# Kernel optimization log

Hardware: AMD Instinct MI355X
Metric: run time of the kernel (lower is better)

Reference implementation:

```python
import jax, jax.numpy as jnp
import numpy as np

D_K = 64
ATTN_MASKED = True
NEG = 1.0e9


def setup_inputs() -> dict:
    key = jax.random.key(0)
    k1, k2, k3, k4 = jax.random.split(key, 4)
    B, H, S, d = 2, 16, 2048, D_K
    Q = jax.random.normal(k1, (B, H, S, d), dtype=jnp.float32)
    K = jax.random.normal(k2, (B, H, S, d), dtype=jnp.float32)
    V = jax.random.normal(k3, (B, H, S, d), dtype=jnp.float32)
    pad_mask = jax.random.randint(k4, (B, S), 0, 2, dtype=jnp.int32)
    return {"Q": Q, "K": K, "V": V, "pad_mask": pad_mask}


def reference(Q, K, V, pad_mask):
    # scores: [B, H, Sq, Sk]
    scores = jnp.einsum("bhqd,bhkd->bhqk", Q, K) / np.sqrt(D_K).astype(np.float32)
    S_out, S_in = scores.shape[-2], scores.shape[-1]
    pad = pad_mask[:, None, None, :].astype(scores.dtype)  # [B,1,1,Sk]
    if ATTN_MASKED:
        causal = jnp.triu(jnp.ones((S_out, S_in), dtype=scores.dtype), k=1)[None, None]
        mask = ((pad + causal) > 0).astype(scores.dtype)
    else:
        mask = jnp.broadcast_to(pad, scores.shape)
    scores = scores - NEG * mask
    attn = jax.nn.softmax(scores, axis=-1)
    return jnp.einsum("bhqk,bhkd->bhqd", attn, V)
```

## Files before the change

### kernel.cpp

```cpp
#include <hip/hip_runtime.h>
#include <hip/hip_bf16.h>

#define S_LEN 2048
#define DH    64
#define NBH   32
#define QT    128
#define KVT   64

typedef __attribute__((ext_vector_type(8)))  short short8;
typedef __attribute__((ext_vector_type(4)))  float f32x4;
typedef __attribute__((ext_vector_type(16))) float f32x16;

static __device__ __forceinline__ unsigned cvtpk_bf16(float a, float b) {
    unsigned r;
    asm("v_cvt_pk_bf16_f32 %0, %1, %2" : "=v"(r) : "v"(a), "v"(b));
    return r;
}

__global__ __launch_bounds__(256)
void attn_fwd(const float* __restrict__ Q, const float* __restrict__ K,
              const float* __restrict__ V, const int* __restrict__ pad,
              float* __restrict__ out)
{
    __shared__ __align__(16) char  ldsK[2][KVT * 128];
    __shared__ __align__(16) char  ldsV[2][DH * 128];
    __shared__ __align__(16) float ldsPB[2][KVT];

    const int tid  = threadIdx.x;
    const int lane = tid & 63;
    const int wid  = tid >> 6;
    const int bx   = gridDim.x - 1 - blockIdx.x;
    const int bh   = blockIdx.y;
    const int b    = bh >> 4;

    const int q0   = bx * QT;
    const int q0w  = q0 + wid * 32;
    const long base = (long)bh * S_LEN * DH;

    const int lq = lane & 31;
    const int hi = lane >> 5;

    const float QS = 0.18033688011112042f;
    short8 bq[4];
    {
        const float* qp = Q + base + (long)(q0w + lq) * DH;
        #pragma unroll
        for (int s = 0; s < 4; ++s) {
            int d0 = s * 16 + hi * 8;
            f32x4 x = *(const f32x4*)(qp + d0);
            f32x4 y = *(const f32x4*)(qp + d0 + 4);
            union { short8 s8; unsigned u[4]; } u;
            u.u[0] = cvtpk_bf16(x[0] * QS, x[1] * QS);
            u.u[1] = cvtpk_bf16(x[2] * QS, x[3] * QS);
            u.u[2] = cvtpk_bf16(y[0] * QS, y[1] * QS);
            u.u[3] = cvtpk_bf16(y[2] * QS, y[3] * QS);
            bq[s] = u.s8;
        }
    }

    f32x16 o0, o1;
    #pragma unroll
    for (int r = 0; r < 16; ++r) { o0[r] = 0.f; o1[r] = 0.f; }
    float m_run = -1e30f, l_run = 0.f;

    const int nkv = 2 * (bx + 1);

    f32x4 kst[4], vst[4];
    int   pst = 0;
    const int vdg = tid & 15, vkq = tid >> 4;
    const float* Kb = K + base;
    const float* Vb = V + base;

    auto stage_load = [&](int t) {
        const float* kp = Kb + t * (KVT * DH);
        #pragma unroll
        for (int i = 0; i < 4; ++i)
            kst[i] = *(const f32x4*)(kp + i * 1024 + tid * 4);
        const float* vp = Vb + t * (KVT * DH);
        #pragma unroll
        for (int j = 0; j < 4; ++j)
            vst[j] = *(const f32x4*)(vp + (vkq * 4 + j) * DH + vdg * 4);
        pst = pad[b * S_LEN + t * KVT + (tid & 63)];
    };
    auto stage_write = [&](int buf) {
        char* kB = ldsK[buf];
        #pragma unroll
        for (int i = 0; i < 4; ++i) {
            int f = i * 1024 + tid * 4;
            int row = f >> 6, dc = f & 63;
            unsigned lo = cvtpk_bf16(kst[i][0], kst[i][1]);
            unsigned h2 = cvtpk_bf16(kst[i][2], kst[i][3]);
            int ch = (dc >> 3) ^ (row & 7);
            *(uint2*)(kB + row * 128 + ch * 16 + (dc & 7) * 2) = make_uint2(lo, h2);
        }
        char* vB = ldsV[buf];
        #pragma unroll
        for (int i = 0; i < 4; ++i) {
            int d = vdg * 4 + i;
            unsigned lo = cvtpk_bf16(vst[0][i], vst[1][i]);
            unsigned h2 = cvtpk_bf16(vst[2][i], vst[3][i]);
            int ch = (vkq >> 1) ^ (d & 7);
            *(uint2*)(vB + d * 128 + ch * 16 + (vkq & 1) * 8) = make_uint2(lo, h2);
        }
        if (tid < KVT) ldsPB[buf][tid] = pst ? -1e30f : 0.f;
    };

    stage_load(0);
    stage_write(0);
    __syncthreads();

    for (int t = 0; t < nkv; ++t) {
        const int cur = t & 1;
        const int kv0 = t * KVT;
        if (t + 1 < nkv) stage_load(t + 1);

        if (kv0 <= q0w + 31) {
            const char*  kB = ldsK[cur];
            const char*  vB = ldsV[cur];
            const float* pb = ldsPB[cur];
            const int    rsw = lq & 7;

            f32x16 s0, s1;
            #pragma unroll
            for (int g = 0; g < 4; ++g) {
                f32x4 p0 = *(const f32x4*)(pb + g * 8 + hi * 4);
                f32x4 p1 = *(const f32x4*)(pb + 32 + g * 8 + hi * 4);
                #pragma unroll
                for (int i = 0; i < 4; ++i) { s0[g * 4 + i] = p0[i]; s1[g * 4 + i] = p1[i]; }
            }

            __builtin_amdgcn_s_setprio(1);
            #pragma unroll
            for (int s = 0; s < 4; ++s) {
                int ch = (((s * 2 + hi) ^ rsw) * 16);
                short8 ak0 = *(const short8*)(kB + lq * 128 + ch);
                short8 ak1 = *(const short8*)(kB + (32 + lq) * 128 + ch);
                s0 = __builtin_amdgcn_mfma_f32_32x32x16_bf16(ak0, bq[s], s0, 0, 0, 0);
                s1 = __builtin_amdgcn_mfma_f32_32x32x16_bf16(ak1, bq[s], s1, 0, 0, 0);
            }
            __builtin_amdgcn_s_setprio(0);

            if (kv0 + 63 > q0w) {
                int q = q0w + lq;
                #pragma unroll
                for (int r = 0; r < 16; ++r) {
                    int key0 = kv0 + (r & 3) + 8 * (r >> 2) + 4 * hi;
                    if (key0 > q)      s0[r] = -1e30f;
                    if (key0 + 32 > q) s1[r] = -1e30f;
                }
            }

            float bm = -1e30f;
            #pragma unroll
            for (int r = 0; r < 16; ++r) bm = fmaxf(bm, fmaxf(s0[r], s1[r]));
            bm = fmaxf(bm, __shfl_xor(bm, 32));
            if (__any(bm > m_run + 8.0f)) {
                float mnew = fmaxf(m_run, bm);
                float c = exp2f(m_run - mnew);
                m_run = mnew;
                l_run *= c;
                #pragma unroll
                for (int r = 0; r < 16; ++r) { o0[r] *= c; o1[r] *= c; }
            }
            float rs = 0.f;
            #pragma unroll
            for (int r = 0; r < 16; ++r) {
                float p0 = exp2f(s0[r] - m_run);
                float p1 = exp2f(s1[r] - m_run);
                s0[r] = p0; s1[r] = p1;
                rs += p0 + p1;
            }
            rs += __shfl_xor(rs, 32);
            l_run += rs;

            short8 pfr[4];
            #pragma unroll
            for (int fs = 0; fs < 4; ++fs) {
                const f32x16& sp = (fs < 2) ? s0 : s1;
                const int rb = (fs & 1) * 8;
                unsigned a0 = cvtpk_bf16(sp[rb + 0], sp[rb + 1]);
                unsigned b0 = cvtpk_bf16(sp[rb + 4], sp[rb + 5]);
                asm("v_permlane32_swap_b32 %0, %1" : "+v"(a0), "+v"(b0));
                unsigned a1 = cvtpk_bf16(sp[rb + 2], sp[rb + 3]);
                unsigned b1 = cvtpk_bf16(sp[rb + 6], sp[rb + 7]);
                asm("v_permlane32_swap_b32 %0, %1" : "+v"(a1), "+v"(b1));
                union { short8 s8; unsigned u[4]; } u;
                u.u[0] = a0; u.u[1] = a1; u.u[2] = b0; u.u[3] = b1;
                pfr[fs] = u.s8;
            }

            __builtin_amdgcn_s_setprio(1);
            #pragma unroll
            for (int fs = 0; fs < 4; ++fs) {
                int ch = (((fs * 2 + hi) ^ rsw) * 16);
                short8 av0 = *(const short8*)(vB + lq * 128 + ch);
                short8 av1 = *(const short8*)(vB + (32 + lq) * 128 + ch);
                o0 = __builtin_amdgcn_mfma_f32_32x32x16_bf16(av0, pfr[fs], o0, 0, 0, 0);
                o1 = __builtin_amdgcn_mfma_f32_32x32x16_bf16(av1, pfr[fs], o1, 0, 0, 0);
            }
            __builtin_amdgcn_s_setprio(0);
        }

        if (t + 1 < nkv) stage_write((t + 1) & 1);
        __syncthreads();
    }

    float invl = 1.0f / l_run;
    float* op = out + base + (long)(q0w + lq) * DH;
    #pragma unroll
    for (int g = 0; g < 4; ++g) {
        f32x4 w0, w1;
        #pragma unroll
        for (int i = 0; i < 4; ++i) {
            w0[i] = o0[g * 4 + i] * invl;
            w1[i] = o1[g * 4 + i] * invl;
        }
        *(f32x4*)(op + g * 8 + hi * 4)      = w0;
        *(f32x4*)(op + 32 + g * 8 + hi * 4) = w1;
    }
}

__global__ void fz_kernel(const int* __restrict__ pad, int* __restrict__ fz)
{
    int b = blockIdx.x;
    __shared__ int red[256];
    int local = S_LEN;
    for (int k = threadIdx.x; k < S_LEN; k += 256)
        if (pad[b * S_LEN + k] == 0 && k < local) local = k;
    red[threadIdx.x] = local;
    __syncthreads();
    for (int s = 128; s > 0; s >>= 1) {
        if (threadIdx.x < s) red[threadIdx.x] = min(red[threadIdx.x], red[threadIdx.x + s]);
        __syncthreads();
    }
    if (threadIdx.x == 0) fz[b] = red[0];
}

__global__ __launch_bounds__(1024)
void meanv_kernel(const float* __restrict__ V, const int* __restrict__ fz,
                  float* __restrict__ meanv)
{
    const int bh = blockIdx.x;
    const int b  = bh >> 4;
    if (fz[b] <= 0) return;

    const int d4 = threadIdx.x & 15;
    const int kp = threadIdx.x >> 4;
    const float* vp = V + (long)bh * S_LEN * DH;

    f32x4 acc = (f32x4){0.f, 0.f, 0.f, 0.f};
    #pragma unroll 4
    for (int k = kp; k < S_LEN; k += 64)
        acc += *(const f32x4*)(vp + (long)k * DH + d4 * 4);

    __shared__ f32x4 red[64][16];
    red[kp][d4] = acc;
    __syncthreads();
    #pragma unroll
    for (int s = 32; s >= 1; s >>= 1) {
        if (kp < s) red[kp][d4] += red[kp + s][d4];
        __syncthreads();
    }
    if (kp == 0) {
        f32x4 m = red[0][d4] * (1.0f / 2048.0f);
        *(f32x4*)(meanv + bh * DH + d4 * 4) = m;
    }
}

__global__ void fixup_kernel(const int* __restrict__ fz, const float* __restrict__ meanv,
                             float* __restrict__ out)
{
    const int bh = blockIdx.x;
    const int b  = bh >> 4;
    const int n  = fz[b];
    if (n <= 0) return;

    __shared__ float mv[DH];
    if (threadIdx.x < DH) mv[threadIdx.x] = meanv[bh * DH + threadIdx.x];
    __syncthreads();

    float* op = out + (long)bh * S_LEN * DH;
    for (int i = threadIdx.x; i < n * DH; i += 256) op[i] = mv[i & 63];
}

extern "C" void kernel_launch(void* const* d_in, const int* in_sizes, int n_in,
                              void* d_out, int out_size, void* d_ws, size_t ws_size,
                              hipStream_t stream)
{
    const float* Q   = (const float*)d_in[0];
    const float* K   = (const float*)d_in[1];
    const float* V   = (const float*)d_in[2];
    const int*   pad = (const int*)d_in[3];
    float* out   = (float*)d_out;
    int*   fz    = (int*)d_ws;
    float* meanv = (float*)((char*)d_ws + 256);

    fz_kernel<<<dim3(2), dim3(256), 0, stream>>>(pad, fz);
    attn_fwd<<<dim3(S_LEN / QT, NBH), dim3(256), 0, stream>>>(Q, K, V, pad, out);
    meanv_kernel<<<dim3(NBH), dim3(1024), 0, stream>>>(V, fz, meanv);
    fixup_kernel<<<dim3(NBH), dim3(256), 0, stream>>>(fz, meanv, out);
}
```

Measured before the change: 107.5 us.

## Pre-convert K/V to swizzled bf16 tiles and stream via global_load_lds

Adds a prep kernel that converts K and V once into bf16 tiles already in the swizzled LDS layout, plus a kernel that precomputes the pad bias. The attention kernel then copies those tiles straight into LDS with global_load_lds instead of loading fp32, converting and writing through registers. It also remaps the grid so heavy and light causal blocks are interleaved. The cost is extra launches, workspace traffic, and a full vmcnt wait before each barrier. It only takes this path when the workspace is large enough, otherwise it falls back to the old kernel.

```diff
diff --git a/kernel.cpp b/kernel.cpp
--- a/kernel.cpp
+++ b/kernel.cpp
@@ -6,6 +6,7 @@
 #define NBH   32
 #define QT    128
 #define KVT   64
+#define NTILE 32
 
 typedef __attribute__((ext_vector_type(8)))  short short8;
 typedef __attribute__((ext_vector_type(4)))  float f32x4;
@@ -17,10 +18,75 @@
     return r;
 }
 
+typedef __attribute__((address_space(1))) const void gvoid_t;
+typedef __attribute__((address_space(3))) void lvoid_t;
+static __device__ __forceinline__ void gload16(const void* g, void* l) {
+    __builtin_amdgcn_global_load_lds((gvoid_t*)g, (lvoid_t*)l, 16, 0, 0);
+}
+static __device__ __forceinline__ void gload4(const void* g, void* l) {
+    __builtin_amdgcn_global_load_lds((gvoid_t*)g, (lvoid_t*)l, 4, 0, 0);
+}
+
 __global__ __launch_bounds__(256)
-void attn_fwd(const float* __restrict__ Q, const float* __restrict__ K,
-              const float* __restrict__ V, const int* __restrict__ pad,
-              float* __restrict__ out)
+void prep_kernel(const float* __restrict__ K, const float* __restrict__ V,
+                 char* __restrict__ Kimg, char* __restrict__ Vimg)
+{
+    const int t   = blockIdx.x;
+    const int bh  = blockIdx.y;
+    const int tid = threadIdx.x;
+    const long tileOff = ((long)bh * NTILE + t) * 8192;
+    const long srcOff  = (long)bh * S_LEN * DH + (long)t * KVT * DH;
+
+    {
+        const float* kp = K + srcOff;
+        char* dst = Kimg + tileOff;
+        #pragma unroll
+        for (int i = 0; i < 4; ++i) {
+            int f = i * 1024 + tid * 4;
+            int row = f >> 6, dc = f & 63;
+            f32x4 x = *(const f32x4*)(kp + f);
+            unsigned lo = cvtpk_bf16(x[0], x[1]);
+            unsigned h2 = cvtpk_bf16(x[2], x[3]);
+            int ch = (dc >> 3) ^ (row & 7);
+            *(uint2*)(dst + row * 128 + ch * 16 + (dc & 7) * 2) = make_uint2(lo, h2);
+        }
+    }
+    {
+        const float* vp = V + srcOff;
+        char* dst = Vimg + tileOff;
+        const int vdg = tid & 15, vkq = tid >> 4;
+        float rv[4][4];
+        #pragma unroll
+        for (int j = 0; j < 4; ++j) {
+            f32x4 x = *(const f32x4*)(vp + (vkq * 4 + j) * DH + vdg * 4);
+            rv[j][0] = x[0]; rv[j][1] = x[1]; rv[j][2] = x[2]; rv[j][3] = x[3];
+        }
+        #pragma unroll
+        for (int i = 0; i < 4; ++i) {
+            int d = vdg * 4 + i;
+            unsigned lo = cvtpk_bf16(rv[0][i], rv[1][i]);
+            unsigned h2 = cvtpk_bf16(rv[2][i], rv[3][i]);
+            int ch = (vkq >> 1) ^ (d & 7);
+            *(uint2*)(dst + d * 128 + ch * 16 + (vkq & 1) * 8) = make_uint2(lo, h2);
+        }
+    }
+}
+
+__global__ __launch_bounds__(1024)
+void bias_kernel(const int* __restrict__ pad, float* __restrict__ bias)
+{
+    int b = blockIdx.x;
+    #pragma unroll
+    for (int i = 0; i < 2; ++i) {
+        int k = threadIdx.x + i * 1024;
+        bias[b * S_LEN + k] = pad[b * S_LEN + k] ? -1e30f : 0.f;
+    }
+}
+
+__global__ __launch_bounds__(256)
+void attn_fwd2(const float* __restrict__ Q, const char* __restrict__ Kimg,
+               const char* __restrict__ Vimg, const float* __restrict__ bias,
+               float* __restrict__ out)
 {
     __shared__ __align__(16) char  ldsK[2][KVT * 128];
     __shared__ __align__(16) char  ldsV[2][DH * 128];
@@ -29,12 +95,15 @@
     const int tid  = threadIdx.x;
     const int lane = tid & 63;
     const int wid  = tid >> 6;
-    const int bx   = gridDim.x - 1 - blockIdx.x;
-    const int bh   = blockIdx.y;
+
+    const int gid  = blockIdx.x;
+    const int half = gid >> 8;
+    const int r    = gid & 255;
+    const int bx   = half ? (r & 15) : 15 - (r & 15);
+    const int bh   = (r >> 4) + (half << 4);
     const int b    = bh >> 4;
 
-    const int q0   = bx * QT;
-    const int q0w  = q0 + wid * 32;
+    const int q0w  = bx * QT + wid * 32;
     const long base = (long)bh * S_LEN * DH;
 
     const int lq = lane & 31;
@@ -60,59 +129,43 @@
 
     f32x16 o0, o1;
     #pragma unroll
-    for (int r = 0; r < 16; ++r) { o0[r] = 0.f; o1[r] = 0.f; }
+    for (int rr = 0; rr < 16; ++rr) { o0[rr] = 0.f; o1[rr] = 0.f; }
     float m_run = -1e30f, l_run = 0.f;
 
     const int nkv = 2 * (bx + 1);
-
-    f32x4 kst[4], vst[4];
-    int   pst = 0;
-    const int vdg = tid & 15, vkq = tid >> 4;
-    const float* Kb = K + base;
-    const float* Vb = V + base;
-
-    auto stage_load = [&](int t) {
-        const float* kp = Kb + t * (KVT * DH);
-        #pragma unroll
-        for (int i = 0; i < 4; ++i)
-            kst[i] = *(const f32x4*)(kp + i * 1024 + tid * 4);
-        const float* vp = Vb + t * (KVT * DH);
-        #pragma unroll
-        for (int j = 0; j < 4; ++j)
-            vst[j] = *(const f32x4*)(vp + (vkq * 4 + j) * DH + vdg * 4);
-        pst = pad[b * S_LEN + t * KVT + (tid & 63)];
+    const char*  KimgB = Kimg + (long)bh * NTILE * 8192;
+    const char*  VimgB = Vimg + (long)bh * NTILE * 8192;
+    const float* biasB = bias + b * S_LEN;
+
+    auto stage = [&](int t, int buf) {
+        if (wid < 2) {
+            const char* src = KimgB + (long)t * 8192 + lane * 16;
+            char* dst = ldsK[buf];
+            #pragma unroll
+            for (int s = 0; s < 4; ++s) {
+                int seg = wid * 4 + s;
+                gload16(src + seg * 1024, dst + seg * 1024);
+            }
+            if (wid == 0) gload4(biasB + t * KVT + lane, ldsPB[buf]);
+        } else {
+            const char* src = VimgB + (long)t * 8192 + lane * 16;
+            char* dst = ldsV[buf];
+            #pragma unroll
+            for (int s = 0; s < 4; ++s) {
+                int seg = (wid - 2) * 4 + s;
+                gload16(src + seg * 1024, dst + seg * 1024);
+            }
+        }
     };
-    auto stage_write = [&](int buf) {
-        char* kB = ldsK[buf];
-        #pragma unroll
-        for (int i = 0; i < 4; ++i) {
-            int f = i * 1024 + tid * 4;
-            int row = f >> 6, dc = f & 63;
-            unsigned lo = cvtpk_bf16(kst[i][0], kst[i][1]);
-            unsigned h2 = cvtpk_bf16(kst[i][2], kst[i][3]);
-            int ch = (dc >> 3) ^ (row & 7);
-            *(uint2*)(kB + row * 128 + ch * 16 + (dc & 7) * 2) = make_uint2(lo, h2);
-        }
-        char* vB = ldsV[buf];
-        #pragma unroll
-        for (int i = 0; i < 4; ++i) {
-            int d = vdg * 4 + i;
-            unsigned lo = cvtpk_bf16(vst[0][i], vst[1][i]);
-            unsigned h2 = cvtpk_bf16(vst[2][i], vst[3][i]);
-            int ch = (vkq >> 1) ^ (d & 7);
-            *(uint2*)(vB + d * 128 + ch * 16 + (vkq & 1) * 8) = make_uint2(lo, h2);
-        }
-        if (tid < KVT) ldsPB[buf][tid] = pst ? -1e30f : 0.f;
-    };
-
-    stage_load(0);
-    stage_write(0);
+
+    stage(0, 0);
+    asm volatile("s_waitcnt vmcnt(0)" ::: "memory");
     __syncthreads();
 
     for (int t = 0; t < nkv; ++t) {
         const int cur = t & 1;
         const int kv0 = t * KVT;
-        if (t + 1 < nkv) stage_load(t + 1);
+        if (t + 1 < nkv) stage(t + 1, cur ^ 1);
 
         if (kv0 <= q0w + 31) {
             const char*  kB = ldsK[cur];
@@ -143,16 +196,16 @@
             if (kv0 + 63 > q0w) {
                 int q = q0w + lq;
                 #pragma unroll
-                for (int r = 0; r < 16; ++r) {
-                    int key0 = kv0 + (r & 3) + 8 * (r >> 2) + 4 * hi;
-                    if (key0 > q)      s0[r] = -1e30f;
-                    if (key0 + 32 > q) s1[r] = -1e30f;
+                for (int rr = 0; rr < 16; ++rr) {
+                    int key0 = kv0 + (rr & 3) + 8 * (rr >> 2) + 4 * hi;
+                    if (key0 > q)      s0[rr] = -1e30f;
+                    if (key0 + 32 > q) s1[rr] = -1e30f;
                 }
             }
 
             float bm = -1e30f;
             #pragma unroll
-            for (int r = 0; r < 16; ++r) bm = fmaxf(bm, fmaxf(s0[r], s1[r]));
+            for (int rr = 0; rr < 16; ++rr) bm = fmaxf(bm, fmaxf(s0[rr], s1[rr]));
             bm = fmaxf(bm, __shfl_xor(bm, 32));
             if (__any(bm > m_run + 8.0f)) {
                 float mnew = fmaxf(m_run, bm);
@@ -160,14 +213,14 @@
                 m_run = mnew;
                 l_run *= c;
                 #pragma unroll
-                for (int r = 0; r < 16; ++r) { o0[r] *= c; o1[r] *= c; }
+                for (int rr = 0; rr < 16; ++rr) { o0[rr] *= c; o1[rr] *= c; }
             }
             float rs = 0.f;
             #pragma unroll
-            for (int r = 0; r < 16; ++r) {
-                float p0 = exp2f(s0[r] - m_run);
-                float p1 = exp2f(s1[r] - m_run);
-                s0[r] = p0; s1[r] = p1;
+            for (int rr = 0; rr < 16; ++rr) {
+                float p0 = exp2f(s0[rr] - m_run);
+                float p1 = exp2f(s1[rr] - m_run);
+                s0[rr] = p0; s1[rr] = p1;
                 rs += p0 + p1;
             }
             rs += __shfl_xor(rs, 32);
@@ -201,6 +254,196 @@
             __builtin_amdgcn_s_setprio(0);
         }
 
+        asm volatile("s_waitcnt vmcnt(0)" ::: "memory");
+        __syncthreads();
+    }
+
+    float invl = 1.0f / l_run;
+    float* op = out + base + (long)(q0w + lq) * DH;
+    #pragma unroll
+    for (int g = 0; g < 4; ++g) {
+        f32x4 w0, w1;
+        #pragma unroll
+        for (int i = 0; i < 4; ++i) {
+            w0[i] = o0[g * 4 + i] * invl;
+            w1[i] = o1[g * 4 + i] * invl;
+        }
+        *(f32x4*)(op + g * 8 + hi * 4)      = w0;
+        *(f32x4*)(op + 32 + g * 8 + hi * 4) = w1;
+    }
+}
+
+__global__ __launch_bounds__(256)
+void attn_fwd(const float* __restrict__ Q, const float* __restrict__ K,
+              const float* __restrict__ V, const int* __restrict__ pad,
+              float* __restrict__ out)
+{
+    __shared__ __align__(16) char  ldsK[2][KVT * 128];
+    __shared__ __align__(16) char  ldsV[2][DH * 128];
+    __shared__ __align__(16) float ldsPB[2][KVT];
+
+    const int tid  = threadIdx.x;
+    const int lane = tid & 63;
+    const int wid  = tid >> 6;
+    const int bx   = gridDim.x - 1 - blockIdx.x;
+    const int bh   = blockIdx.y;
+    const int b    = bh >> 4;
+
+    const int q0w  = bx * QT + wid * 32;
+    const long base = (long)bh * S_LEN * DH;
+    const int lq = lane & 31;
+    const int hi = lane >> 5;
+
+    const float QS = 0.18033688011112042f;
+    short8 bq[4];
+    {
+        const float* qp = Q + base + (long)(q0w + lq) * DH;
+        #pragma unroll
+        for (int s = 0; s < 4; ++s) {
+            int d0 = s * 16 + hi * 8;
+            f32x4 x = *(const f32x4*)(qp + d0);
+            f32x4 y = *(const f32x4*)(qp + d0 + 4);
+            union { short8 s8; unsigned u[4]; } u;
+            u.u[0] = cvtpk_bf16(x[0] * QS, x[1] * QS);
+            u.u[1] = cvtpk_bf16(x[2] * QS, x[3] * QS);
+            u.u[2] = cvtpk_bf16(y[0] * QS, y[1] * QS);
+            u.u[3] = cvtpk_bf16(y[2] * QS, y[3] * QS);
+            bq[s] = u.s8;
+        }
+    }
+
+    f32x16 o0, o1;
+    #pragma unroll
+    for (int rr = 0; rr < 16; ++rr) { o0[rr] = 0.f; o1[rr] = 0.f; }
+    float m_run = -1e30f, l_run = 0.f;
+
+    const int nkv = 2 * (bx + 1);
+    f32x4 kst[4], vst[4];
+    int   pst = 0;
+    const int vdg = tid & 15, vkq = tid >> 4;
+    const float* Kb = K + base;
+    const float* Vb = V + base;
+
+    auto stage_load = [&](int t) {
+        const float* kp = Kb + t * (KVT * DH);
+        #pragma unroll
+        for (int i = 0; i < 4; ++i) kst[i] = *(const f32x4*)(kp + i * 1024 + tid * 4);
+        const float* vp = Vb + t * (KVT * DH);
+        #pragma unroll
+        for (int j = 0; j < 4; ++j) vst[j] = *(const f32x4*)(vp + (vkq * 4 + j) * DH + vdg * 4);
+        pst = pad[b * S_LEN + t * KVT + (tid & 63)];
+    };
+    auto stage_write = [&](int buf) {
+        char* kB = ldsK[buf];
+        #pragma unroll
+        for (int i = 0; i < 4; ++i) {
+            int f = i * 1024 + tid * 4;
+            int row = f >> 6, dc = f & 63;
+            unsigned lo = cvtpk_bf16(kst[i][0], kst[i][1]);
+            unsigned h2 = cvtpk_bf16(kst[i][2], kst[i][3]);
+            int ch = (dc >> 3) ^ (row & 7);
+            *(uint2*)(kB + row * 128 + ch * 16 + (dc & 7) * 2) = make_uint2(lo, h2);
+        }
+        char* vB = ldsV[buf];
+        #pragma unroll
+        for (int i = 0; i < 4; ++i) {
+            int d = vdg * 4 + i;
+            unsigned lo = cvtpk_bf16(vst[0][i], vst[1][i]);
+            unsigned h2 = cvtpk_bf16(vst[2][i], vst[3][i]);
+            int ch = (vkq >> 1) ^ (d & 7);
+            *(uint2*)(vB + d * 128 + ch * 16 + (vkq & 1) * 8) = make_uint2(lo, h2);
+        }
+        if (tid < KVT) ldsPB[buf][tid] = pst ? -1e30f : 0.f;
+    };
+
+    stage_load(0);
+    stage_write(0);
+    __syncthreads();
+
+    for (int t = 0; t < nkv; ++t) {
+        const int cur = t & 1;
+        const int kv0 = t * KVT;
+        if (t + 1 < nkv) stage_load(t + 1);
+
+        if (kv0 <= q0w + 31) {
+            const char*  kB = ldsK[cur];
+            const char*  vB = ldsV[cur];
+            const float* pb = ldsPB[cur];
+            const int    rsw = lq & 7;
+            f32x16 s0, s1;
+            #pragma unroll
+            for (int g = 0; g < 4; ++g) {
+                f32x4 p0 = *(const f32x4*)(pb + g * 8 + hi * 4);
+                f32x4 p1 = *(const f32x4*)(pb + 32 + g * 8 + hi * 4);
+                #pragma unroll
+                for (int i = 0; i < 4; ++i) { s0[g * 4 + i] = p0[i]; s1[g * 4 + i] = p1[i]; }
+            }
+            __builtin_amdgcn_s_setprio(1);
+            #pragma unroll
+            for (int s = 0; s < 4; ++s) {
+                int ch = (((s * 2 + hi) ^ rsw) * 16);
+                short8 ak0 = *(const short8*)(kB + lq * 128 + ch);
+                short8 ak1 = *(const short8*)(kB + (32 + lq) * 128 + ch);
+                s0 = __builtin_amdgcn_mfma_f32_32x32x16_bf16(ak0, bq[s], s0, 0, 0, 0);
+                s1 = __builtin_amdgcn_mfma_f32_32x32x16_bf16(ak1, bq[s], s1, 0, 0, 0);
+            }
+            __builtin_amdgcn_s_setprio(0);
+            if (kv0 + 63 > q0w) {
+                int q = q0w + lq;
+                #pragma unroll
+                for (int rr = 0; rr < 16; ++rr) {
+                    int key0 = kv0 + (rr & 3) + 8 * (rr >> 2) + 4 * hi;
+                    if (key0 > q)      s0[rr] = -1e30f;
+                    if (key0 + 32 > q) s1[rr] = -1e30f;
+                }
+            }
+            float bm = -1e30f;
+            #pragma unroll
+            for (int rr = 0; rr < 16; ++rr) bm = fmaxf(bm, fmaxf(s0[rr], s1[rr]));
+            bm = fmaxf(bm, __shfl_xor(bm, 32));
+            if (__any(bm > m_run + 8.0f)) {
+                float mnew = fmaxf(m_run, bm);
+                float c = exp2f(m_run - mnew);
+                m_run = mnew; l_run *= c;
+                #pragma unroll
+                for (int rr = 0; rr < 16; ++rr) { o0[rr] *= c; o1[rr] *= c; }
+            }
+            float rs = 0.f;
+            #pragma unroll
+            for (int rr = 0; rr < 16; ++rr) {
+                float p0 = exp2f(s0[rr] - m_run);
+                float p1 = exp2f(s1[rr] - m_run);
+                s0[rr] = p0; s1[rr] = p1;
+                rs += p0 + p1;
+            }
+            rs += __shfl_xor(rs, 32);
+            l_run += rs;
+            short8 pfr[4];
+            #pragma unroll
+            for (int fs = 0; fs < 4; ++fs) {
+                const f32x16& sp = (fs < 2) ? s0 : s1;
+                const int rb = (fs & 1) * 8;
+                unsigned a0 = cvtpk_bf16(sp[rb + 0], sp[rb + 1]);
+                unsigned b0 = cvtpk_bf16(sp[rb + 4], sp[rb + 5]);
+                asm("v_permlane32_swap_b32 %0, %1" : "+v"(a0), "+v"(b0));
+                unsigned a1 = cvtpk_bf16(sp[rb + 2], sp[rb + 3]);
+                unsigned b1 = cvtpk_bf16(sp[rb + 6], sp[rb + 7]);
+                asm("v_permlane32_swap_b32 %0, %1" : "+v"(a1), "+v"(b1));
+                union { short8 s8; unsigned u[4]; } u;
+                u.u[0] = a0; u.u[1] = a1; u.u[2] = b0; u.u[3] = b1;
+                pfr[fs] = u.s8;
+            }
+            __builtin_amdgcn_s_setprio(1);
+            #pragma unroll
+            for (int fs = 0; fs < 4; ++fs) {
+                int ch = (((fs * 2 + hi) ^ rsw) * 16);
+                short8 av0 = *(const short8*)(vB + lq * 128 + ch);
+                short8 av1 = *(const short8*)(vB + (32 + lq) * 128 + ch);
+                o0 = __builtin_amdgcn_mfma_f32_32x32x16_bf16(av0, pfr[fs], o0, 0, 0, 0);
+                o1 = __builtin_amdgcn_mfma_f32_32x32x16_bf16(av1, pfr[fs], o1, 0, 0, 0);
+            }
+            __builtin_amdgcn_s_setprio(0);
+        }
         if (t + 1 < nkv) stage_write((t + 1) & 1);
         __syncthreads();
     }
@@ -243,16 +486,13 @@
     const int bh = blockIdx.x;
     const int b  = bh >> 4;
     if (fz[b] <= 0) return;
-
     const int d4 = threadIdx.x & 15;
     const int kp = threadIdx.x >> 4;
     const float* vp = V + (long)bh * S_LEN * DH;
-
     f32x4 acc = (f32x4){0.f, 0.f, 0.f, 0.f};
     #pragma unroll 4
     for (int k = kp; k < S_LEN; k += 64)
         acc += *(const f32x4*)(vp + (long)k * DH + d4 * 4);
-
     __shared__ f32x4 red[64][16];
     red[kp][d4] = acc;
     __syncthreads();
@@ -261,10 +501,8 @@
         if (kp < s) red[kp][d4] += red[kp + s][d4];
         __syncthreads();
     }
-    if (kp == 0) {
-        f32x4 m = red[0][d4] * (1.0f / 2048.0f);
-        *(f32x4*)(meanv + bh * DH + d4 * 4) = m;
-    }
+    if (kp == 0)
+        *(f32x4*)(meanv + bh * DH + d4 * 4) = red[0][d4] * (1.0f / 2048.0f);
 }
 
 __global__ void fixup_kernel(const int* __restrict__ fz, const float* __restrict__ meanv,
@@ -274,11 +512,9 @@
     const int b  = bh >> 4;
     const int n  = fz[b];
     if (n <= 0) return;
-
     __shared__ float mv[DH];
     if (threadIdx.x < DH) mv[threadIdx.x] = meanv[bh * DH + threadIdx.x];
     __syncthreads();
-
     float* op = out + (long)bh * S_LEN * DH;
     for (int i = threadIdx.x; i < n * DH; i += 256) op[i] = mv[i & 63];
 }
@@ -292,11 +528,22 @@
     const float* V   = (const float*)d_in[2];
     const int*   pad = (const int*)d_in[3];
     float* out   = (float*)d_out;
+
     int*   fz    = (int*)d_ws;
     float* meanv = (float*)((char*)d_ws + 256);
+    float* bias  = (float*)((char*)d_ws + 8448);
+    char*  Kimg  = (char*)d_ws + 32768;
+    char*  Vimg  = Kimg + (size_t)NBH * NTILE * 8192;
+    const size_t need = 32768 + 2 * (size_t)NBH * NTILE * 8192;
 
     fz_kernel<<<dim3(2), dim3(256), 0, stream>>>(pad, fz);
-    attn_fwd<<<dim3(S_LEN / QT, NBH), dim3(256), 0, stream>>>(Q, K, V, pad, out);
+    if (ws_size >= need) {
+        bias_kernel<<<dim3(2), dim3(1024), 0, stream>>>(pad, bias);
+        prep_kernel<<<dim3(NTILE, NBH), dim3(256), 0, stream>>>(K, V, Kimg, Vimg);
+        attn_fwd2<<<dim3(512), dim3(256), 0, stream>>>(Q, Kimg, Vimg, bias, out);
+    } else {
+        attn_fwd<<<dim3(S_LEN / QT, NBH), dim3(256), 0, stream>>>(Q, K, V, pad, out);
+    }
     meanv_kernel<<<dim3(NBH), dim3(1024), 0, stream>>>(V, fz, meanv);
     fixup_kernel<<<dim3(NBH), dim3(256), 0, stream>>>(fz, meanv, out);
 }
```

New measurement: 91.69 us. 1.17x faster.
